# Kernel tuning notes

Hardware: AMD Instinct MI355X
Metric: run time of the kernel (lower is better)

## Reference

```python
import jax, jax.numpy as jnp
import numpy as np

N, R, K = 4, 16384, 96


def setup_inputs() -> dict:
    key = jax.random.key(0)
    k1, k2, k3 = jax.random.split(key, 3)
    rgbs = jax.random.uniform(k1, (N, R, K, 3), dtype=jnp.float32)
    sigmas = jax.random.normal(k2, (N, R, K, 1), dtype=jnp.float32)
    # depths must be monotonically increasing along K (ray sample depths in [0.5, 3.5])
    depths = jnp.sort(0.5 + 3.0 * jax.random.uniform(k3, (N, R, K, 1), dtype=jnp.float32), axis=2)
    return {"rgbs": rgbs, "sigmas": sigmas, "depths": depths}


def reference(rgbs, sigmas, depths):
    # Default rendering_options: use_max_depth=False, no_dist=False,
    # use_mid_point=True, clamp_mode='mipnerf', last_back=False,
    # normalize_rgb=False, normalize_depth=True, clip_depth=True, white_back=False.
    deltas = depths[:, :, 1:] - depths[:, :, :-1]                  # [N,R,K-1,1]
    # midpoint averaging
    rgbs_m = 0.5 * (rgbs[:, :, :-1] + rgbs[:, :, 1:])              # [N,R,K-1,3]
    sigmas_m = 0.5 * (sigmas[:, :, :-1] + sigmas[:, :, 1:])        # [N,R,K-1,1]
    depths_m = 0.5 * (depths[:, :, :-1] + depths[:, :, 1:])        # [N,R,K-1,1]
    # mipnerf clamp: softplus(sigma - 1)
    sig = jax.nn.softplus(sigmas_m - 1.0)
    alphas = 1.0 - jnp.exp(-deltas * sig)                          # [N,R,K-1,1]
    # transmittance via exclusive cumprod along the sample axis
    alphas_shifted = jnp.concatenate(
        [jnp.ones_like(alphas[:, :, :1]), 1.0 - alphas + 1e-10], axis=-2)
    trans = jnp.cumprod(alphas_shifted, axis=-2)[:, :, :-1]        # [N,R,K-1,1]
    weights = alphas * trans                                       # [N,R,K-1,1]
    weights_sum = weights.sum(axis=2)                              # [N,R,1]
    composite_rgb = jnp.sum(weights * rgbs_m, axis=-2)             # [N,R,3]
    composite_depth = jnp.sum(weights * depths_m, axis=-2)         # [N,R,1]
    # normalize_depth=True
    composite_depth = composite_depth / weights_sum
    # clip_depth=True
    composite_depth = jnp.nan_to_num(composite_depth, nan=jnp.inf)
    composite_depth = jnp.clip(composite_depth, depths_m.min(), depths_m.max())
    composite_rgb = composite_rgb * 2.0 - 1.0
    return composite_rgb, composite_depth, weights
```

## Files before the change

### kernel.cpp

```cpp
#include <hip/hip_runtime.h>
#include <math.h>

#define NRAYS   65536
#define KSAMP   96
#define KM1     95
#define RPB     4
#define RGB_OFF   0
#define DEPTH_OFF (NRAYS * 3)
#define W_OFF     (NRAYS * 3 + NRAYS)

__device__ __forceinline__ float one_minus_alpha(float x, float delta) {
    const float L2E = 1.44269504088896340736f;
    float xl = x * L2E;
    float l2 = (x > 20.0f) ? xl
                           : __builtin_amdgcn_logf(1.0f + __builtin_amdgcn_exp2f(xl));
    return __builtin_amdgcn_exp2f(-delta * l2);
}

__global__ __launch_bounds__(256) void integrate_kernel(
    const float* __restrict__ rgbs,
    const float* __restrict__ sigmas,
    const float* __restrict__ depths,
    float* __restrict__ out)
{
    __shared__ float sh_d[RPB * KSAMP];
    __shared__ float sh_s[RPB * KSAMP];
    __shared__ float sh_rgb[RPB * KSAMP * 3];

    const int tid  = threadIdx.x;
    const int ray0 = blockIdx.x * RPB;

    {
        const float4* gd = (const float4*)(depths + (size_t)ray0 * KSAMP);
        const float4* gs = (const float4*)(sigmas + (size_t)ray0 * KSAMP);
        const float4* gr = (const float4*)(rgbs   + (size_t)ray0 * KSAMP * 3);
        float4* sd4 = (float4*)sh_d;
        float4* ss4 = (float4*)sh_s;
        float4* sr4 = (float4*)sh_rgb;
        if (tid < 96) { sd4[tid] = gd[tid]; ss4[tid] = gs[tid]; }
        sr4[tid] = gr[tid];
        if (tid < 32) sr4[256 + tid] = gr[256 + tid];
    }
    __syncthreads();

    const int wave = tid >> 6;
    const int lane = tid & 63;
    const int ray  = ray0 + wave;
    const float* d  = sh_d   + wave * KSAMP;
    const float* s  = sh_s   + wave * KSAMP;
    const float* rg = sh_rgb + wave * KSAMP * 3;

    const int i0 = 2 * lane;
    const bool v0 = (i0     < KM1);
    const bool v1 = (i0 + 1 < KM1);

    float a0 = 0.f, a1 = 0.f, om0 = 1.f, om1 = 1.f;
    float dm0 = 0.f, dm1 = 0.f;
    float rm00 = 0.f, rm01 = 0.f, rm02 = 0.f;
    float rm10 = 0.f, rm11 = 0.f, rm12 = 0.f;

    if (v0) {
        float dA = d[i0], dB = d[i0 + 1];
        float delta = dB - dA;
        float x = 0.5f * (s[i0] + s[i0 + 1]) - 1.0f;
        float e = one_minus_alpha(x, delta);
        a0 = 1.f - e;
        om0 = e + 1e-10f;
        dm0 = 0.5f * (dA + dB);
        rm00 = 0.5f * (rg[3*i0 + 0] + rg[3*i0 + 3]);
        rm01 = 0.5f * (rg[3*i0 + 1] + rg[3*i0 + 4]);
        rm02 = 0.5f * (rg[3*i0 + 2] + rg[3*i0 + 5]);
    }
    if (v1) {
        int i1 = i0 + 1;
        float dA = d[i1], dB = d[i1 + 1];
        float delta = dB - dA;
        float x = 0.5f * (s[i1] + s[i1 + 1]) - 1.0f;
        float e = one_minus_alpha(x, delta);
        a1 = 1.f - e;
        om1 = e + 1e-10f;
        dm1 = 0.5f * (dA + dB);
        rm10 = 0.5f * (rg[3*i1 + 0] + rg[3*i1 + 3]);
        rm11 = 0.5f * (rg[3*i1 + 1] + rg[3*i1 + 4]);
        rm12 = 0.5f * (rg[3*i1 + 2] + rg[3*i1 + 5]);
    }

    float incl = om0 * om1;
    #pragma unroll
    for (int off = 1; off < 64; off <<= 1) {
        float u = __shfl_up(incl, off);
        if (lane >= off) incl *= u;
    }
    float excl = __shfl_up(incl, 1);
    if (lane == 0) excl = 1.f;

    float w0 = v0 ? a0 * excl : 0.f;
    float w1 = v1 ? a1 * (excl * om0) : 0.f;

    float* wout = out + W_OFF + (size_t)ray * KM1;
    if (v0) wout[i0]     = w0;
    if (v1) wout[i0 + 1] = w1;

    float wsum = w0 + w1;
    float rsum = w0 * rm00 + w1 * rm10;
    float gsum = w0 * rm01 + w1 * rm11;
    float bsum = w0 * rm02 + w1 * rm12;
    float dsum = w0 * dm0  + w1 * dm1;
    #pragma unroll
    for (int off = 32; off; off >>= 1) {
        wsum += __shfl_xor(wsum, off);
        rsum += __shfl_xor(rsum, off);
        gsum += __shfl_xor(gsum, off);
        bsum += __shfl_xor(bsum, off);
        dsum += __shfl_xor(dsum, off);
    }

    if (lane == 0) {
        out[RGB_OFF + (size_t)ray * 3 + 0] = 2.f * rsum - 1.f;
        out[RGB_OFF + (size_t)ray * 3 + 1] = 2.f * gsum - 1.f;
        out[RGB_OFF + (size_t)ray * 3 + 2] = 2.f * bsum - 1.f;

        float dv = dsum / wsum;
        float lo = 0.5f * (d[0]  + d[1]);
        float hi = 0.5f * (d[94] + d[95]);
        dv = fmaxf(fminf(dv, hi), lo);
        out[DEPTH_OFF + ray] = dv;
    }
}

extern "C" void kernel_launch(void* const* d_in, const int* in_sizes, int n_in,
                              void* d_out, int out_size, void* d_ws, size_t ws_size,
                              hipStream_t stream) {
    const float* rgbs   = (const float*)d_in[0];
    const float* sigmas = (const float*)d_in[1];
    const float* depths = (const float*)d_in[2];
    float* out = (float*)d_out;

    integrate_kernel<<<NRAYS / RPB, 256, 0, stream>>>(rgbs, sigmas, depths, out);
}
```

Before: 159.4 us.

## Assign 4 threads per ray with serial segment scans, drop shared memory staging

Instead of one wave per ray staging data through LDS, each ray is split into four 24-sample segments handled by four lanes. Each lane loads its segment directly from global memory with float4 loads, computes a local transmittance product and weighted sums serially, then combines segments with a short shuffle scan and reduction. Weights are written with vector stores. This removes the LDS round-trip, the barrier and the 64-lane scan, but uses more registers per thread and makes global loads strided per lane.

```diff
diff --git a/kernel.cpp b/kernel.cpp
--- a/kernel.cpp
+++ b/kernel.cpp
@@ -1,13 +1,13 @@
 #include <hip/hip_runtime.h>
 #include <math.h>
 
-#define NRAYS   65536
-#define KSAMP   96
-#define KM1     95
-#define RPB     4
+#define NRAYS     65536
+#define KM1       95
 #define RGB_OFF   0
 #define DEPTH_OFF (NRAYS * 3)
-#define W_OFF     (NRAYS * 3 + NRAYS)
+#define W_OFF     (NRAYS * 4)
+
+typedef float f4u __attribute__((ext_vector_type(4), aligned(4)));
 
 __device__ __forceinline__ float one_minus_alpha(float x, float delta) {
     const float L2E = 1.44269504088896340736f;
@@ -23,109 +23,110 @@
     const float* __restrict__ depths,
     float* __restrict__ out)
 {
-    __shared__ float sh_d[RPB * KSAMP];
-    __shared__ float sh_s[RPB * KSAMP];
-    __shared__ float sh_rgb[RPB * KSAMP * 3];
+    const int t   = threadIdx.x;
+    const int seg = t & 3;
+    const int ray = blockIdx.x * 64 + (t >> 2);
 
-    const int tid  = threadIdx.x;
-    const int ray0 = blockIdx.x * RPB;
+    const float* db = depths + ray * 96  + seg * 24;
+    const float* sb = sigmas + ray * 96  + seg * 24;
+    const float* rb = rgbs   + ray * 288 + seg * 72;
 
-    {
-        const float4* gd = (const float4*)(depths + (size_t)ray0 * KSAMP);
-        const float4* gs = (const float4*)(sigmas + (size_t)ray0 * KSAMP);
-        const float4* gr = (const float4*)(rgbs   + (size_t)ray0 * KSAMP * 3);
-        float4* sd4 = (float4*)sh_d;
-        float4* ss4 = (float4*)sh_s;
-        float4* sr4 = (float4*)sh_rgb;
-        if (tid < 96) { sd4[tid] = gd[tid]; ss4[tid] = gs[tid]; }
-        sr4[tid] = gr[tid];
-        if (tid < 32) sr4[256 + tid] = gr[256 + tid];
-    }
-    __syncthreads();
+    float u[24];
+    float Tloc = 1.0f;
+    float Sw = 0.f, Sd = 0.f, Sr = 0.f, Sg = 0.f, Sb = 0.f;
+    float d0f=0.f, s0f=0.f, r0f=0.f, g0f=0.f, b0f=0.f, d1f=0.f, dpen=0.f;
+    float dp=0.f, sp=0.f, rp=0.f, gp=0.f, bp=0.f;
 
-    const int wave = tid >> 6;
-    const int lane = tid & 63;
-    const int ray  = ray0 + wave;
-    const float* d  = sh_d   + wave * KSAMP;
-    const float* s  = sh_s   + wave * KSAMP;
-    const float* rg = sh_rgb + wave * KSAMP * 3;
+#define DO_IV(IDX, dA,sA,rA,gA,bA, dB,sB,rB,gB,bB)                 \
+    { float delta = (dB) - (dA);                                   \
+      float x = 0.5f * ((sA) + (sB)) - 1.0f;                       \
+      float e = one_minus_alpha(x, delta);                         \
+      float uu = (1.0f - e) * Tloc;                                \
+      Tloc *= e + 1e-10f;                                          \
+      u[IDX] = uu;                                                 \
+      Sw += uu;                                                    \
+      Sd += uu * (0.5f * ((dA) + (dB)));                           \
+      Sr += uu * (0.5f * ((rA) + (rB)));                           \
+      Sg += uu * (0.5f * ((gA) + (gB)));                           \
+      Sb += uu * (0.5f * ((bA) + (bB))); }
 
-    const int i0 = 2 * lane;
-    const bool v0 = (i0     < KM1);
-    const bool v1 = (i0 + 1 < KM1);
-
-    float a0 = 0.f, a1 = 0.f, om0 = 1.f, om1 = 1.f;
-    float dm0 = 0.f, dm1 = 0.f;
-    float rm00 = 0.f, rm01 = 0.f, rm02 = 0.f;
-    float rm10 = 0.f, rm11 = 0.f, rm12 = 0.f;
-
-    if (v0) {
-        float dA = d[i0], dB = d[i0 + 1];
-        float delta = dB - dA;
-        float x = 0.5f * (s[i0] + s[i0 + 1]) - 1.0f;
-        float e = one_minus_alpha(x, delta);
-        a0 = 1.f - e;
-        om0 = e + 1e-10f;
-        dm0 = 0.5f * (dA + dB);
-        rm00 = 0.5f * (rg[3*i0 + 0] + rg[3*i0 + 3]);
-        rm01 = 0.5f * (rg[3*i0 + 1] + rg[3*i0 + 4]);
-        rm02 = 0.5f * (rg[3*i0 + 2] + rg[3*i0 + 5]);
-    }
-    if (v1) {
-        int i1 = i0 + 1;
-        float dA = d[i1], dB = d[i1 + 1];
-        float delta = dB - dA;
-        float x = 0.5f * (s[i1] + s[i1 + 1]) - 1.0f;
-        float e = one_minus_alpha(x, delta);
-        a1 = 1.f - e;
-        om1 = e + 1e-10f;
-        dm1 = 0.5f * (dA + dB);
-        rm10 = 0.5f * (rg[3*i1 + 0] + rg[3*i1 + 3]);
-        rm11 = 0.5f * (rg[3*i1 + 1] + rg[3*i1 + 4]);
-        rm12 = 0.5f * (rg[3*i1 + 2] + rg[3*i1 + 5]);
+    #pragma unroll
+    for (int j = 0; j < 6; ++j) {
+        float4 d4 = *(const float4*)(db + 4*j);
+        float4 s4 = *(const float4*)(sb + 4*j);
+        float4 r0 = *(const float4*)(rb + 12*j);
+        float4 r1 = *(const float4*)(rb + 12*j + 4);
+        float4 r2 = *(const float4*)(rb + 12*j + 8);
+        if (j == 0) {
+            d0f=d4.x; s0f=s4.x; r0f=r0.x; g0f=r0.y; b0f=r0.z; d1f=d4.y;
+        } else {
+            DO_IV(4*j-1, dp,sp,rp,gp,bp, d4.x,s4.x,r0.x,r0.y,r0.z);
+        }
+        DO_IV(4*j+0, d4.x,s4.x,r0.x,r0.y,r0.z,  d4.y,s4.y,r0.w,r1.x,r1.y);
+        DO_IV(4*j+1, d4.y,s4.y,r0.w,r1.x,r1.y,  d4.z,s4.z,r1.z,r1.w,r2.x);
+        DO_IV(4*j+2, d4.z,s4.z,r1.z,r1.w,r2.x,  d4.w,s4.w,r2.y,r2.z,r2.w);
+        if (j == 5) dpen = d4.z;
+        dp=d4.w; sp=s4.w; rp=r2.y; gp=r2.z; bp=r2.w;
     }
 
-    float incl = om0 * om1;
-    #pragma unroll
-    for (int off = 1; off < 64; off <<= 1) {
-        float u = __shfl_up(incl, off);
-        if (lane >= off) incl *= u;
-    }
-    float excl = __shfl_up(incl, 1);
-    if (lane == 0) excl = 1.f;
-
-    float w0 = v0 ? a0 * excl : 0.f;
-    float w1 = v1 ? a1 * (excl * om0) : 0.f;
-
-    float* wout = out + W_OFF + (size_t)ray * KM1;
-    if (v0) wout[i0]     = w0;
-    if (v1) wout[i0 + 1] = w1;
-
-    float wsum = w0 + w1;
-    float rsum = w0 * rm00 + w1 * rm10;
-    float gsum = w0 * rm01 + w1 * rm11;
-    float bsum = w0 * rm02 + w1 * rm12;
-    float dsum = w0 * dm0  + w1 * dm1;
-    #pragma unroll
-    for (int off = 32; off; off >>= 1) {
-        wsum += __shfl_xor(wsum, off);
-        rsum += __shfl_xor(rsum, off);
-        gsum += __shfl_xor(gsum, off);
-        bsum += __shfl_xor(bsum, off);
-        dsum += __shfl_xor(dsum, off);
+    float dn = __shfl_down(d0f, 1);
+    float sn = __shfl_down(s0f, 1);
+    float rn = __shfl_down(r0f, 1);
+    float gn = __shfl_down(g0f, 1);
+    float bn = __shfl_down(b0f, 1);
+    if (seg < 3) {
+        DO_IV(23, dp,sp,rp,gp,bp, dn,sn,rn,gn,bn);
+    } else {
+        u[23] = 0.0f;
     }
 
-    if (lane == 0) {
-        out[RGB_OFF + (size_t)ray * 3 + 0] = 2.f * rsum - 1.f;
-        out[RGB_OFF + (size_t)ray * 3 + 1] = 2.f * gsum - 1.f;
-        out[RGB_OFF + (size_t)ray * 3 + 2] = 2.f * bsum - 1.f;
+    float incl = Tloc;
+    float p1 = __shfl_up(incl, 1); if (seg >= 1) incl *= p1;
+    float p2 = __shfl_up(incl, 2); if (seg >= 2) incl *= p2;
+    float Tin = __shfl_up(incl, 1);
+    if (seg == 0) Tin = 1.0f;
 
-        float dv = dsum / wsum;
-        float lo = 0.5f * (d[0]  + d[1]);
-        float hi = 0.5f * (d[94] + d[95]);
+    Sw *= Tin; Sd *= Tin; Sr *= Tin; Sg *= Tin; Sb *= Tin;
+    #pragma unroll
+    for (int off = 1; off <= 2; off <<= 1) {
+        Sw += __shfl_xor(Sw, off);
+        Sd += __shfl_xor(Sd, off);
+        Sr += __shfl_xor(Sr, off);
+        Sg += __shfl_xor(Sg, off);
+        Sb += __shfl_xor(Sb, off);
+    }
+
+    float* wout = out + W_OFF + ray * 95 + seg * 24;
+    if (seg < 3) {
+        #pragma unroll
+        for (int k = 0; k < 6; ++k) {
+            f4u v = { Tin*u[4*k], Tin*u[4*k+1], Tin*u[4*k+2], Tin*u[4*k+3] };
+            *(f4u*)(wout + 4*k) = v;
+        }
+    } else {
+        #pragma unroll
+        for (int k = 0; k < 5; ++k) {
+            f4u v = { Tin*u[4*k], Tin*u[4*k+1], Tin*u[4*k+2], Tin*u[4*k+3] };
+            *(f4u*)(wout + 4*k) = v;
+        }
+        wout[20] = Tin*u[20];
+        wout[21] = Tin*u[21];
+        wout[22] = Tin*u[22];
+    }
+
+    float hiloc = 0.5f * (dpen + dp);
+    const int lane = t & 63;
+    float hi = __shfl(hiloc, lane | 3);
+    if (seg == 0) {
+        out[RGB_OFF + ray*3 + 0] = 2.f*Sr - 1.f;
+        out[RGB_OFF + ray*3 + 1] = 2.f*Sg - 1.f;
+        out[RGB_OFF + ray*3 + 2] = 2.f*Sb - 1.f;
+        float dv = Sd / Sw;
+        float lo = 0.5f * (d0f + d1f);
         dv = fmaxf(fminf(dv, hi), lo);
         out[DEPTH_OFF + ray] = dv;
     }
+#undef DO_IV
 }
 
 extern "C" void kernel_launch(void* const* d_in, const int* in_sizes, int n_in,
@@ -136,5 +137,5 @@
     const float* depths = (const float*)d_in[2];
     float* out = (float*)d_out;
 
-    integrate_kernel<<<NRAYS / RPB, 256, 0, stream>>>(rgbs, sigmas, depths, out);
+    integrate_kernel<<<NRAYS / 64, 256, 0, stream>>>(rgbs, sigmas, depths, out);
 }
```

Measured after the change: 177.8 us. +11.6%, slower.
